# Performance work log

Hardware: AMD Instinct MI355X
Metric: run time of the kernel (lower is better)

The kernel has to match this reference:

```python
import jax, jax.numpy as jnp
import numpy as np

B, N, A, RNN, DW, DS = 64, 2048, 512, 1024, 1024, 1024


def setup_inputs() -> dict:
    key = jax.random.key(0)
    ks = jax.random.split(key, 8)
    return {
        "h": jax.random.normal(ks[0], (B, RNN), dtype=jnp.float32),
        "senti_feats": jax.random.normal(ks[1], (B, DS), dtype=jnp.float32),
        "senti_word_feats": jax.random.normal(ks[2], (B, N, DW), dtype=jnp.float32),
        "p_senti_word_feats": jax.random.normal(ks[3], (B, N, A), dtype=jnp.float32),
        "W_h2word": jax.random.normal(ks[4], (A, RNN), dtype=jnp.float32) * 0.03,
        "b_h2word": jax.random.normal(ks[5], (A,), dtype=jnp.float32) * 0.03,
        "w_alpha": jax.random.normal(ks[6], (A,), dtype=jnp.float32) * 0.03,
        "b_alpha": jnp.zeros((), dtype=jnp.float32),
    }


def reference(h, senti_feats, senti_word_feats, p_senti_word_feats,
              W_h2word, b_h2word, w_alpha, b_alpha):
    # h_word: [B, A]
    h_word = h @ W_h2word.T + b_h2word
    # additive attention scores: [B, N]
    act = jnp.tanh(p_senti_word_feats + h_word[:, None, :])
    scores = jnp.einsum('bna,a->bn', act, w_alpha) + b_alpha
    weight = jax.nn.softmax(scores, axis=-1)
    # weighted sum pooling over N: [B, DW]
    word_res = jnp.einsum('bn,bnd->bd', weight, senti_word_feats)
    return jnp.concatenate([senti_feats, word_res], axis=-1)
```

## Files before the change

### kernel.cpp

```cpp
#include <hip/hip_runtime.h>
#include <math.h>

#define B   64
#define N   2048
#define A   512
#define RNN 1024
#define DW  1024
#define DS  1024
#define NCHUNK 16
#define CHUNK  (N / NCHUNK)

__device__ __forceinline__ float wave_reduce_sum(float v) {
    #pragma unroll
    for (int off = 32; off > 0; off >>= 1)
        v += __shfl_down(v, off, 64);
    return v;
}

__device__ __forceinline__ float fast_tanh(float x) {
    float e = __builtin_amdgcn_exp2f(x * 2.8853900817779268f);
    return 1.0f - 2.0f * __builtin_amdgcn_rcpf(e + 1.0f);
}

__global__ __launch_bounds__(256) void k_hword(const float* __restrict__ h,
                                               const float* __restrict__ W,
                                               const float* __restrict__ bias,
                                               float* __restrict__ hword) {
    __shared__ float4 hs[RNN / 4];
    const int b   = blockIdx.x;
    const int tid = threadIdx.x;
    const float4* h4 = (const float4*)(h + (size_t)b * RNN);
    for (int i = tid; i < RNN / 4; i += 256) hs[i] = h4[i];
    __syncthreads();
    const int wave = tid >> 6, lane = tid & 63;
    const int a0 = blockIdx.y * 128;
    for (int i = wave; i < 128; i += 4) {
        const int a = a0 + i;
        const float4* w4 = (const float4*)(W + (size_t)a * RNN);
        float acc = 0.f;
        #pragma unroll
        for (int j = 0; j < 4; ++j) {
            const int k4 = lane + 64 * j;
            float4 wv = w4[k4];
            float4 hv = hs[k4];
            acc += wv.x * hv.x + wv.y * hv.y + wv.z * hv.z + wv.w * hv.w;
        }
        acc = wave_reduce_sum(acc);
        if (lane == 0) hword[b * A + a] = acc + bias[a];
    }
}

__global__ __launch_bounds__(256) void k_scores(const float* __restrict__ p,
                                                const float* __restrict__ hword,
                                                const float* __restrict__ walpha,
                                                const float* __restrict__ balpha,
                                                float* __restrict__ scores) {
    const int wave = threadIdx.x >> 6, lane = threadIdx.x & 63;
    const int row  = blockIdx.x * 4 + wave;
    const int b    = row >> 11;
    const float4* p4 = (const float4*)(p + (size_t)row * A);
    const float4* h4 = (const float4*)(hword + (size_t)b * A);
    const float4* w4 = (const float4*)walpha;
    float acc = 0.f;
    #pragma unroll
    for (int j = 0; j < 2; ++j) {
        const int k4 = lane + 64 * j;
        float4 pv = p4[k4];
        float4 hv = h4[k4];
        float4 wv = w4[k4];
        acc += fast_tanh(pv.x + hv.x) * wv.x;
        acc += fast_tanh(pv.y + hv.y) * wv.y;
        acc += fast_tanh(pv.z + hv.z) * wv.z;
        acc += fast_tanh(pv.w + hv.w) * wv.w;
    }
    acc = wave_reduce_sum(acc);
    if (lane == 0) scores[row] = acc + balpha[0];
}

__global__ __launch_bounds__(256) void k_softmax(float* __restrict__ sw) {
    const int b   = blockIdx.x;
    float* row = sw + (size_t)b * N;
    const int tid = threadIdx.x;
    const int wave = tid >> 6, lane = tid & 63;
    float v[8];
    float m = -1e30f;
    #pragma unroll
    for (int i = 0; i < 8; ++i) { v[i] = row[tid + 256 * i]; m = fmaxf(m, v[i]); }
    __shared__ float redm[4];
    #pragma unroll
    for (int off = 32; off > 0; off >>= 1) m = fmaxf(m, __shfl_down(m, off, 64));
    if (lane == 0) redm[wave] = m;
    __syncthreads();
    m = fmaxf(fmaxf(redm[0], redm[1]), fmaxf(redm[2], redm[3]));
    float s = 0.f;
    #pragma unroll
    for (int i = 0; i < 8; ++i) {
        v[i] = __builtin_amdgcn_exp2f((v[i] - m) * 1.4426950408889634f);
        s += v[i];
    }
    s = wave_reduce_sum(s);
    __shared__ float reds[4];
    if (lane == 0) reds[wave] = s;
    __syncthreads();
    s = reds[0] + reds[1] + reds[2] + reds[3];
    const float inv = __builtin_amdgcn_rcpf(s);
    #pragma unroll
    for (int i = 0; i < 8; ++i) row[tid + 256 * i] = v[i] * inv;
}

__global__ __launch_bounds__(256) void k_pool(const float* __restrict__ swf,
                                              const float* __restrict__ weight,
                                              float* __restrict__ partial) {
    const int b  = blockIdx.x;
    const int c  = blockIdx.y;
    const int n0 = c * CHUNK;
    const int t  = threadIdx.x;
    const float4* s4 = (const float4*)swf + ((size_t)b * N + n0) * (DW / 4) + t;
    const float* w   = weight + (size_t)b * N + n0;
    float4 acc = make_float4(0.f, 0.f, 0.f, 0.f);
    #pragma unroll 4
    for (int n = 0; n < CHUNK; ++n) {
        const float wv = w[n];
        float4 v = s4[(size_t)n * (DW / 4)];
        acc.x += wv * v.x; acc.y += wv * v.y; acc.z += wv * v.z; acc.w += wv * v.w;
    }
    ((float4*)partial)[((size_t)b * NCHUNK + c) * (DW / 4) + t] = acc;
}

__global__ __launch_bounds__(256) void k_reduce_concat(const float* __restrict__ senti,
                                                       const float* __restrict__ partial,
                                                       float* __restrict__ out) {
    const int b = blockIdx.x;
    const int t = threadIdx.x;
    float4* o4 = (float4*)out + (size_t)b * ((DS + DW) / 4);
    o4[t] = ((const float4*)senti)[(size_t)b * (DS / 4) + t];
    const float4* p4 = (const float4*)partial + (size_t)b * NCHUNK * (DW / 4) + t;
    float4 acc = make_float4(0.f, 0.f, 0.f, 0.f);
    #pragma unroll
    for (int c = 0; c < NCHUNK; ++c) {
        float4 v = p4[(size_t)c * (DW / 4)];
        acc.x += v.x; acc.y += v.y; acc.z += v.z; acc.w += v.w;
    }
    o4[DS / 4 + t] = acc;
}

extern "C" void kernel_launch(void* const* d_in, const int* in_sizes, int n_in,
                              void* d_out, int out_size, void* d_ws, size_t ws_size,
                              hipStream_t stream) {
    const float* h      = (const float*)d_in[0];
    const float* senti  = (const float*)d_in[1];
    const float* swf    = (const float*)d_in[2];
    const float* p      = (const float*)d_in[3];
    const float* W      = (const float*)d_in[4];
    const float* bh     = (const float*)d_in[5];
    const float* walpha = (const float*)d_in[6];
    const float* balpha = (const float*)d_in[7];
    float* out = (float*)d_out;
    float* ws  = (float*)d_ws;

    float* hword   = ws;
    float* sw      = hword + B * A;
    float* partial = sw + B * N;

    k_hword        <<<dim3(B, 4),      256, 0, stream>>>(h, W, bh, hword);
    k_scores       <<<dim3(B * N / 4), 256, 0, stream>>>(p, hword, walpha, balpha, sw);
    k_softmax      <<<dim3(B),         256, 0, stream>>>(sw);
    k_pool         <<<dim3(B, NCHUNK), 256, 0, stream>>>(swf, sw, partial);
    k_reduce_concat<<<dim3(B),         256, 0, stream>>>(senti, partial, out);
}
```

Before: 855.1 us.

## Fuse softmax into pooling kernel and double pooling chunk count

Drops the separate softmax kernel. Each pooling block now recomputes the row max and sum over all N scores, then normalizes only its own chunk's weights into shared memory. NCHUNK is raised from 16 to 32, which gives more blocks for the bandwidth-bound weighted sum. The cost is redundant softmax reductions per block and a larger partial buffer for the final reduce, in exchange for one fewer launch and no write/read round trip for the weights.

```diff
diff --git a/kernel.cpp b/kernel.cpp
--- a/kernel.cpp
+++ b/kernel.cpp
@@ -7,7 +7,7 @@
 #define RNN 1024
 #define DW  1024
 #define DS  1024
-#define NCHUNK 16
+#define NCHUNK 32
 #define CHUNK  (N / NCHUNK)
 
 __device__ __forceinline__ float wave_reduce_sum(float v) {
@@ -77,16 +77,20 @@
     if (lane == 0) scores[row] = acc + balpha[0];
 }
 
-__global__ __launch_bounds__(256) void k_softmax(float* __restrict__ sw) {
-    const int b   = blockIdx.x;
-    float* row = sw + (size_t)b * N;
-    const int tid = threadIdx.x;
-    const int wave = tid >> 6, lane = tid & 63;
+__global__ __launch_bounds__(256) void k_pool(const float* __restrict__ swf,
+                                              const float* __restrict__ scores,
+                                              float* __restrict__ partial) {
+    const int b = blockIdx.x;
+    const int c = blockIdx.y;
+    const int t = threadIdx.x;
+    const int wave = t >> 6, lane = t & 63;
+    const float* srow = scores + (size_t)b * N;
+
     float v[8];
     float m = -1e30f;
     #pragma unroll
-    for (int i = 0; i < 8; ++i) { v[i] = row[tid + 256 * i]; m = fmaxf(m, v[i]); }
-    __shared__ float redm[4];
+    for (int i = 0; i < 8; ++i) { v[i] = srow[t + 256 * i]; m = fmaxf(m, v[i]); }
+    __shared__ float redm[4], reds[4];
     #pragma unroll
     for (int off = 32; off > 0; off >>= 1) m = fmaxf(m, __shfl_down(m, off, 64));
     if (lane == 0) redm[wave] = m;
@@ -94,35 +98,27 @@
     m = fmaxf(fmaxf(redm[0], redm[1]), fmaxf(redm[2], redm[3]));
     float s = 0.f;
     #pragma unroll
-    for (int i = 0; i < 8; ++i) {
-        v[i] = __builtin_amdgcn_exp2f((v[i] - m) * 1.4426950408889634f);
-        s += v[i];
-    }
+    for (int i = 0; i < 8; ++i)
+        s += __builtin_amdgcn_exp2f((v[i] - m) * 1.4426950408889634f);
     s = wave_reduce_sum(s);
-    __shared__ float reds[4];
     if (lane == 0) reds[wave] = s;
     __syncthreads();
     s = reds[0] + reds[1] + reds[2] + reds[3];
     const float inv = __builtin_amdgcn_rcpf(s);
-    #pragma unroll
-    for (int i = 0; i < 8; ++i) row[tid + 256 * i] = v[i] * inv;
-}
 
-__global__ __launch_bounds__(256) void k_pool(const float* __restrict__ swf,
-                                              const float* __restrict__ weight,
-                                              float* __restrict__ partial) {
-    const int b  = blockIdx.x;
-    const int c  = blockIdx.y;
+    __shared__ float wl[CHUNK];
     const int n0 = c * CHUNK;
-    const int t  = threadIdx.x;
+    if (t < CHUNK)
+        wl[t] = __builtin_amdgcn_exp2f((srow[n0 + t] - m) * 1.4426950408889634f) * inv;
+    __syncthreads();
+
     const float4* s4 = (const float4*)swf + ((size_t)b * N + n0) * (DW / 4) + t;
-    const float* w   = weight + (size_t)b * N + n0;
     float4 acc = make_float4(0.f, 0.f, 0.f, 0.f);
     #pragma unroll 4
     for (int n = 0; n < CHUNK; ++n) {
-        const float wv = w[n];
-        float4 v = s4[(size_t)n * (DW / 4)];
-        acc.x += wv * v.x; acc.y += wv * v.y; acc.z += wv * v.z; acc.w += wv * v.w;
+        const float wv = wl[n];
+        float4 x = s4[(size_t)n * (DW / 4)];
+        acc.x += wv * x.x; acc.y += wv * x.y; acc.z += wv * x.z; acc.w += wv * x.w;
     }
     ((float4*)partial)[((size_t)b * NCHUNK + c) * (DW / 4) + t] = acc;
 }
@@ -162,9 +158,8 @@
     float* sw      = hword + B * A;
     float* partial = sw + B * N;
 
-    k_hword        <<<dim3(B, 4),      256, 0, stream>>>(h, W, bh, hword);
-    k_scores       <<<dim3(B * N / 4), 256, 0, stream>>>(p, hword, walpha, balpha, sw);
-    k_softmax      <<<dim3(B),         256, 0, stream>>>(sw);
-    k_pool         <<<dim3(B, NCHUNK), 256, 0, stream>>>(swf, sw, partial);
-    k_reduce_concat<<<dim3(B),         256, 0, stream>>>(senti, partial, out);
+    k_hword        <<<dim3(B, 4),       256, 0, stream>>>(h, W, bh, hword);
+    k_scores       <<<dim3(B * N / 4),  256, 0, stream>>>(p, hword, walpha, balpha, sw);
+    k_pool         <<<dim3(B, NCHUNK),  256, 0, stream>>>(swf, sw, partial);
+    k_reduce_concat<<<dim3(B),          256, 0, stream>>>(senti, partial, out);
 }
```

New measurement: 859.5 us. Within noise of the previous version (+0.5%).
